# Kernel optimization log

Measured on AMD Instinct MI355X. Metric: run time of the kernel, lower is better.

## Reference

```python
import jax, jax.numpy as jnp
import numpy as np

IMG_H, IMG_W = 16, 16
N = IMG_H * IMG_W              # 256 tokens
HEADS = 8
HEAD_DIM = 32
INNER = HEADS * HEAD_DIM       # 256
IN_CH = 256
OUT_CH = 256
BATCH = 64
SCALE = HEAD_DIM ** -0.5


def _make_relative_index():
    # Mirrors the torch buffer construction exactly.
    coords = np.stack(np.meshgrid(np.arange(IMG_H), np.arange(IMG_W), indexing='ij'))
    coords = coords.reshape(2, -1)                      # (2, N)
    rel = coords[:, :, None] - coords[:, None, :]       # (2, N, N)
    rel[0] += IMG_H - 1
    rel[1] += IMG_W - 1
    rel[0] *= 2 * IMG_W - 1
    idx = rel.sum(0).reshape(-1)                        # (N*N,) values in [0, (2H-1)(2W-1))
    return idx.astype(np.int32)


def setup_inputs() -> dict:
    key = jax.random.key(0)
    k1, k2, k3, k4, k5 = jax.random.split(key, 5)
    x = jax.random.normal(k1, (BATCH, N, IN_CH), dtype=jnp.float32)
    w_qkv = jax.random.normal(k2, (IN_CH, 3 * INNER), dtype=jnp.float32) * 0.02
    bias_table = jax.random.normal(k3, ((2 * IMG_H - 1) * (2 * IMG_W - 1), HEADS), dtype=jnp.float32) * 0.02
    w_out = jax.random.normal(k4, (INNER, OUT_CH), dtype=jnp.float32) * 0.02
    b_out = jax.random.normal(k5, (OUT_CH,), dtype=jnp.float32) * 0.02
    rel_index = jnp.asarray(_make_relative_index())
    return {"x": x, "w_qkv": w_qkv, "bias_table": bias_table,
            "w_out": w_out, "b_out": b_out, "rel_index": rel_index}


def reference(x, w_qkv, bias_table, w_out, b_out, rel_index):
    b, n, _ = x.shape
    qkv = x @ w_qkv                                     # (b, n, 3*inner)
    q, k, v = jnp.split(qkv, 3, axis=-1)
    def heads(t):
        return t.reshape(b, n, HEADS, HEAD_DIM).transpose(0, 2, 1, 3)  # (b, h, n, d)
    q, k, v = heads(q), heads(k), heads(v)
    dots = jnp.einsum('bhid,bhjd->bhij', q, k) * SCALE  # (b, h, n, n)
    # gather relative position bias: (n*n, h) -> (1, h, n, n)
    rel_bias = bias_table[rel_index].reshape(n, n, HEADS).transpose(2, 0, 1)[None]
    attn = jax.nn.softmax(dots + rel_bias, axis=-1)
    out = jnp.einsum('bhij,bhjd->bhid', attn, v)        # (b, h, n, d)
    out = out.transpose(0, 2, 1, 3).reshape(b, n, INNER)
    return out @ w_out + b_out
```

## Files before the change

kernel.cpp:

```cpp
#include <hip/hip_runtime.h>
#include <hip/hip_bf16.h>

typedef __bf16 bfv8 __attribute__((ext_vector_type(8)));
typedef float f32x4 __attribute__((ext_vector_type(4)));
typedef unsigned short u16;
typedef unsigned int u32;
typedef u16 u16x8 __attribute__((ext_vector_type(8)));

__device__ __forceinline__ float bf2f(u16 u){ union{u32 i; float f;} x; x.i=(u32)u<<16; return x.f; }
__device__ __forceinline__ u16 f2bf(float f){ union{float f; u32 i;} x; x.f=f; u32 i=x.i; return (u16)((i + 0x7FFFu + ((i>>16)&1u))>>16); }

__device__ __forceinline__ void gl16(const void* g, void* l){
  __builtin_amdgcn_global_load_lds((const __attribute__((address_space(1))) unsigned int*)g,
                                   (__attribute__((address_space(3))) unsigned int*)l, 16, 0, 0);
}

__global__ __launch_bounds__(256) void prep_k(const float* __restrict__ x, u16* __restrict__ xb,
                                              const float* __restrict__ w_qkv, u16* __restrict__ wT,
                                              const float* __restrict__ w_out, u16* __restrict__ woT,
                                              const float* __restrict__ bt, const int* __restrict__ ridx,
                                              u16* __restrict__ biasp2){
  __shared__ u16 tile[32][34];
  const int bid = blockIdx.x, tid = threadIdx.x;
  if (bid < 2048){
    int i = (bid*256 + tid)*8;
    float4 a = *(const float4*)&x[i];
    float4 b = *(const float4*)&x[i+4];
    u16 r[8] = { f2bf(a.x),f2bf(a.y),f2bf(a.z),f2bf(a.w), f2bf(b.x),f2bf(b.y),f2bf(b.z),f2bf(b.w) };
    *(int4*)&xb[i] = *(int4*)r;
  } else if (bid < 2048+192){
    int b2 = bid - 2048;
    int c0 = (b2 % 24)*32, r0 = (b2/24)*32;
    int tx = tid & 31, ty = tid >> 5;
    #pragma unroll
    for(int dy=0; dy<32; dy+=8) tile[ty+dy][tx] = f2bf(w_qkv[(size_t)(r0+ty+dy)*768 + (c0+tx)]);
    __syncthreads();
    #pragma unroll
    for(int dy=0; dy<32; dy+=8) wT[(size_t)(c0+ty+dy)*256 + (r0+tx)] = tile[tx][ty+dy];
  } else if (bid < 2048+192+64){
    int b3 = bid - (2048+192);
    int c0 = (b3 & 7)*32, r0 = (b3 >> 3)*32;
    int tx = tid & 31, ty = tid >> 5;
    #pragma unroll
    for(int dy=0; dy<32; dy+=8) tile[ty+dy][tx] = f2bf(w_out[(size_t)(r0+ty+dy)*256 + (c0+tx)]);
    __syncthreads();
    #pragma unroll
    for(int dy=0; dy<32; dy+=8) woT[(size_t)(c0+ty+dy)*256 + (r0+tx)] = tile[tx][ty+dy];
  } else {
    const float L2E = 1.4426950408889634f;
    int idx = (bid - (2048+192+64))*256 + tid;
    int e = idx & 7, ch = (idx>>3)&7, lane = (idx>>6)&63, rb = (idx>>12)&15, h = (idx>>16)&7;
    int ll = lane & 15, lg = lane >> 4;
    int tj = ch*2 + (e>>2), r = e & 3;
    int q = rb*16 + ll, k = 16*tj + 4*lg + r;
    biasp2[idx] = f2bf(bt[ridx[q*256 + k]*8 + h] * L2E);
  }
}

template<bool BIAS, typename OUT, int TM>
__global__ __launch_bounds__(256) void gemm_k(const u16* __restrict__ A, const u16* __restrict__ Bt,
                         const float* __restrict__ bias, OUT* __restrict__ C, int M, int N, int K){
  constexpr int MI = TM/32;
  __shared__ u16 As[TM*64];
  __shared__ u16 Bs[128*64];
  const int tid = threadIdx.x, lane = tid & 63, wv = tid >> 6;
  const int lg = lane >> 4, ll = lane & 15;
  const int wr = (wv >> 1)*(TM/2), wc = (wv & 1)*64;
  const size_t m0 = (size_t)blockIdx.x*TM;
  const int n0 = blockIdx.y*128;
  const int lrow = lane >> 3, lcol = (lane & 7)*8;
  f32x4 acc[MI][4] = {};
  for(int k0=0; k0<K; k0+=64){
    #pragma unroll
    for(int c=0;c<MI;++c){
      int rowbase = (wv*MI + c)*8;
      gl16(&A[(m0 + rowbase + lrow)*(size_t)K + k0 + lcol], &As[rowbase*64]);
    }
    #pragma unroll
    for(int c=0;c<4;++c){
      int rowbase = (wv*4 + c)*8;
      gl16(&Bt[(size_t)(n0 + rowbase + lrow)*K + k0 + lcol], &Bs[rowbase*64]);
    }
    __syncthreads();
    bfv8 af[MI][2], bf[4][2];
    #pragma unroll
    for(int i=0;i<MI;++i)
      #pragma unroll
      for(int kh=0;kh<2;++kh) af[i][kh] = *(const bfv8*)&As[(wr+16*i+ll)*64 + kh*32 + lg*8];
    #pragma unroll
    for(int j=0;j<4;++j)
      #pragma unroll
      for(int kh=0;kh<2;++kh) bf[j][kh] = *(const bfv8*)&Bs[(wc+16*j+ll)*64 + kh*32 + lg*8];
    #pragma unroll
    for(int kh=0;kh<2;++kh)
      #pragma unroll
      for(int i=0;i<MI;++i)
        #pragma unroll
        for(int j=0;j<4;++j)
          acc[i][j] = __builtin_amdgcn_mfma_f32_16x16x32_bf16(af[i][kh], bf[j][kh], acc[i][j], 0,0,0);
    __syncthreads();
  }
  #pragma unroll
  for(int i=0;i<MI;++i)
    #pragma unroll
    for(int j=0;j<4;++j){
      int col = n0 + wc + 16*j + ll;
      float bv = 0.f;
      if (BIAS) bv = bias[col];
      #pragma unroll
      for(int r=0;r<4;++r){
        size_t row = m0 + wr + 16*i + lg*4 + r;
        float v = acc[i][j][r] + bv;
        if constexpr (sizeof(OUT) == 2) C[row*(size_t)N + col] = f2bf(v);
        else                            C[row*(size_t)N + col] = v;
      }
    }
}

__global__ __launch_bounds__(512) void attn_k(const u16* __restrict__ qkv, const u16* __restrict__ biasp2, u16* __restrict__ attnb){
  __shared__ u16 Ks[256*40];
  __shared__ u16 Vt[32*264];
  const int i = blockIdx.x;
  const int b = i & 63, h = i >> 6;
  const int tid = threadIdx.x, lane = tid & 63, wv = tid >> 6;
  const int lg = lane >> 4, ll = lane & 15;
  const u16* qb = qkv + (size_t)b*256*768;
  #pragma unroll
  for(int p=0;p<2;++p){
    int ch = tid + p*512;
    int j = ch >> 2, d8 = (ch & 3)*8;
    *(int4*)&Ks[j*40 + d8] = *(const int4*)&qb[(size_t)j*768 + 256 + h*32 + d8];
  }
  #pragma unroll
  for(int it=0; it<8; ++it){
    int e = tid + it*512;
    int j = e >> 4, dp = (e & 15)*2;
    int jp = ((j>>5)<<5) + 8*((j>>2)&3) + 4*((j>>4)&1) + (j&3);
    u32 v = *(const u32*)&qb[(size_t)j*768 + 512 + h*32 + dp];
    Vt[dp*264 + jp]     = (u16)(v & 0xffffu);
    Vt[(dp+1)*264 + jp] = (u16)(v >> 16);
  }
  __syncthreads();
  const float SCALE2 = 0.17677669529663687f * 1.4426950408889634f;
  const f32x4 zero = {0.f,0.f,0.f,0.f};
  #pragma unroll 1
  for(int iter=0; iter<2; ++iter){
    const int q0 = iter*128 + wv*16;
    const u16* bp = biasp2 + ((((size_t)h*16 + (q0>>4))*64 + lane) << 6);
    u16x8 bias[8];
    #pragma unroll
    for(int g=0; g<8; ++g) bias[g] = *(const u16x8*)&bp[g*8];
    bfv8 qf = *(const bfv8*)&qb[(size_t)(q0+ll)*768 + h*32 + lg*8];
    f32x4 s[16];
    #pragma unroll
    for(int tj=0;tj<16;++tj){
      bfv8 kf = *(const bfv8*)&Ks[(16*tj+ll)*40 + lg*8];
      s[tj] = __builtin_amdgcn_mfma_f32_16x16x32_bf16(kf, qf, zero, 0,0,0);
    }
    f32x4 sm = {0.f,0.f,0.f,0.f};
    #pragma unroll
    for(int tj=0;tj<16;++tj){
      #pragma unroll
      for(int r=0;r<4;++r){
        float p = exp2f(fmaf(s[tj][r], SCALE2, bf2f(bias[tj>>1][4*(tj&1)+r])));
        s[tj][r] = p;
        sm[r] += p;
      }
    }
    float sum = sm[0]+sm[1]+sm[2]+sm[3];
    sum += __shfl_xor(sum,16);
    sum += __shfl_xor(sum,32);
    float rinv = 1.0f/sum;
    u32 pk[16][2];
    #pragma unroll
    for(int tj=0;tj<16;++tj){
      asm("v_cvt_pk_bf16_f32 %0, %1, %2" : "=v"(pk[tj][0]) : "v"(s[tj][0]), "v"(s[tj][1]));
      asm("v_cvt_pk_bf16_f32 %0, %1, %2" : "=v"(pk[tj][1]) : "v"(s[tj][2]), "v"(s[tj][3]));
    }
    f32x4 o[2] = {zero, zero};
    #pragma unroll
    for(int c=0;c<8;++c){
      union { u32 u[4]; bfv8 v; } pu;
      pu.u[0] = pk[2*c][0]; pu.u[1] = pk[2*c][1]; pu.u[2] = pk[2*c+1][0]; pu.u[3] = pk[2*c+1][1];
      bfv8 pf = pu.v;
      #pragma unroll
      for(int td=0;td<2;++td){
        bfv8 vf = *(const bfv8*)&Vt[(16*td+ll)*264 + 32*c + lg*8];
        o[td] = __builtin_amdgcn_mfma_f32_16x16x32_bf16(pf, vf, o[td], 0,0,0);
      }
    }
    #pragma unroll
    for(int td=0;td<2;++td)
      #pragma unroll
      for(int r=0;r<4;++r){
        float rl = __shfl(rinv, 4*lg + r);
        int row = q0 + 4*lg + r;
        attnb[((size_t)b*256 + row)*256 + h*32 + 16*td + ll] = f2bf(o[td][r]*rl);
      }
  }
}

extern "C" void kernel_launch(void* const* d_in, const int* in_sizes, int n_in,
                              void* d_out, int out_size, void* d_ws, size_t ws_size,
                              hipStream_t stream) {
  const float* x     = (const float*)d_in[0];
  const float* w_qkv = (const float*)d_in[1];
  const float* btab  = (const float*)d_in[2];
  const float* w_out = (const float*)d_in[3];
  const float* b_out = (const float*)d_in[4];
  const int*   ridx  = (const int*)d_in[5];
  float* out = (float*)d_out;

  char* ws = (char*)d_ws;
  size_t off = 0;
  u16*   xb     = (u16*)(ws + off); off += (size_t)64*256*256*2;
  u16*   wT     = (u16*)(ws + off); off += (size_t)768*256*2;
  u16*   woT    = (u16*)(ws + off); off += (size_t)256*256*2;
  u16*   biasp2 = (u16*)(ws + off); off += (size_t)524288*2;
  u16*   qkvb   = (u16*)(ws + off); off += (size_t)64*256*768*2;
  u16*   attnb  = (u16*)(ws + off); off += (size_t)64*256*256*2;

  prep_k<<<2048+192+64+2048,256,0,stream>>>(x, xb, w_qkv, wT, w_out, woT, btab, ridx, biasp2);
  gemm_k<false,u16,64><<<dim3(256,6),256,0,stream>>>(xb, wT, nullptr, qkvb, 16384, 768, 256);
  attn_k<<<512,512,0,stream>>>(qkvb, biasp2, attnb);
  gemm_k<true,float,32><<<dim3(512,2),256,0,stream>>>(attnb, woT, b_out, out, 16384, 256, 256);
}
```

Baseline: 56.66 us.

## Compute softmax row sums via MFMA with ones and prefetch bias/Q before K/V staging

The attention kernel now issues the global loads for both query tiles' bias and Q fragments before staging K and V into shared memory, so their latency overlaps the LDS fill. The softmax denominator is taken from an extra MFMA against a vector of bf16 ones instead of a VALU sum plus cross-lane shuffles, which also makes it use the same bf16-rounded probabilities as the PV product. It adds s_setprio around the MFMA phases and sets a minimum-blocks launch bound. The cost is extra registers for the doubled prefetched state and a possible occupancy or spill risk from the launch bound.

Measured after the change: 61.95 us. 1.09x slower.

```diff
diff --git a/kernel.cpp b/kernel.cpp
--- a/kernel.cpp
+++ b/kernel.cpp
@@ -117,7 +117,7 @@
     }
 }
 
-__global__ __launch_bounds__(512) void attn_k(const u16* __restrict__ qkv, const u16* __restrict__ biasp2, u16* __restrict__ attnb){
+__global__ __launch_bounds__(512,4) void attn_k(const u16* __restrict__ qkv, const u16* __restrict__ biasp2, u16* __restrict__ attnb){
   __shared__ u16 Ks[256*40];
   __shared__ u16 Vt[32*264];
   const int i = blockIdx.x;
@@ -125,6 +125,14 @@
   const int tid = threadIdx.x, lane = tid & 63, wv = tid >> 6;
   const int lg = lane >> 4, ll = lane & 15;
   const u16* qb = qkv + (size_t)b*256*768;
+  const int q00 = wv*16, q01 = 128 + wv*16;
+  const u16* bp0 = biasp2 + ((((size_t)h*16 + (q00>>4))*64 + lane) << 6);
+  const u16* bp1 = biasp2 + ((((size_t)h*16 + (q01>>4))*64 + lane) << 6);
+  u16x8 bias0[8], bias1[8];
+  #pragma unroll
+  for(int g=0; g<8; ++g){ bias0[g] = *(const u16x8*)&bp0[g*8]; bias1[g] = *(const u16x8*)&bp1[g*8]; }
+  bfv8 qf0 = *(const bfv8*)&qb[(size_t)(q00+ll)*768 + h*32 + lg*8];
+  bfv8 qf1 = *(const bfv8*)&qb[(size_t)(q01+ll)*768 + h*32 + lg*8];
   #pragma unroll
   for(int p=0;p<2;++p){
     int ch = tid + p*512;
@@ -143,34 +151,23 @@
   __syncthreads();
   const float SCALE2 = 0.17677669529663687f * 1.4426950408889634f;
   const f32x4 zero = {0.f,0.f,0.f,0.f};
-  #pragma unroll 1
-  for(int iter=0; iter<2; ++iter){
-    const int q0 = iter*128 + wv*16;
-    const u16* bp = biasp2 + ((((size_t)h*16 + (q0>>4))*64 + lane) << 6);
-    u16x8 bias[8];
-    #pragma unroll
-    for(int g=0; g<8; ++g) bias[g] = *(const u16x8*)&bp[g*8];
-    bfv8 qf = *(const bfv8*)&qb[(size_t)(q0+ll)*768 + h*32 + lg*8];
+  union { u16 u[8]; bfv8 v; } one8;
+  #pragma unroll
+  for(int t=0;t<8;++t) one8.u[t] = 0x3F80;
+  auto process = [&](int q0, const u16x8* bias, bfv8 qf){
     f32x4 s[16];
+    __builtin_amdgcn_s_setprio(1);
     #pragma unroll
     for(int tj=0;tj<16;++tj){
       bfv8 kf = *(const bfv8*)&Ks[(16*tj+ll)*40 + lg*8];
       s[tj] = __builtin_amdgcn_mfma_f32_16x16x32_bf16(kf, qf, zero, 0,0,0);
     }
-    f32x4 sm = {0.f,0.f,0.f,0.f};
-    #pragma unroll
-    for(int tj=0;tj<16;++tj){
-      #pragma unroll
-      for(int r=0;r<4;++r){
-        float p = exp2f(fmaf(s[tj][r], SCALE2, bf2f(bias[tj>>1][4*(tj&1)+r])));
-        s[tj][r] = p;
-        sm[r] += p;
-      }
-    }
-    float sum = sm[0]+sm[1]+sm[2]+sm[3];
-    sum += __shfl_xor(sum,16);
-    sum += __shfl_xor(sum,32);
-    float rinv = 1.0f/sum;
+    __builtin_amdgcn_s_setprio(0);
+    #pragma unroll
+    for(int tj=0;tj<16;++tj)
+      #pragma unroll
+      for(int r=0;r<4;++r)
+        s[tj][r] = exp2f(fmaf(s[tj][r], SCALE2, bf2f(bias[tj>>1][4*(tj&1)+r])));
     u32 pk[16][2];
     #pragma unroll
     for(int tj=0;tj<16;++tj){
@@ -178,6 +175,8 @@
       asm("v_cvt_pk_bf16_f32 %0, %1, %2" : "=v"(pk[tj][1]) : "v"(s[tj][2]), "v"(s[tj][3]));
     }
     f32x4 o[2] = {zero, zero};
+    f32x4 o2 = zero;
+    __builtin_amdgcn_s_setprio(1);
     #pragma unroll
     for(int c=0;c<8;++c){
       union { u32 u[4]; bfv8 v; } pu;
@@ -188,16 +187,19 @@
         bfv8 vf = *(const bfv8*)&Vt[(16*td+ll)*264 + 32*c + lg*8];
         o[td] = __builtin_amdgcn_mfma_f32_16x16x32_bf16(pf, vf, o[td], 0,0,0);
       }
-    }
-    #pragma unroll
-    for(int td=0;td<2;++td)
-      #pragma unroll
-      for(int r=0;r<4;++r){
-        float rl = __shfl(rinv, 4*lg + r);
-        int row = q0 + 4*lg + r;
-        attnb[((size_t)b*256 + row)*256 + h*32 + 16*td + ll] = f2bf(o[td][r]*rl);
-      }
-  }
+      o2 = __builtin_amdgcn_mfma_f32_16x16x32_bf16(pf, one8.v, o2, 0,0,0);
+    }
+    __builtin_amdgcn_s_setprio(0);
+    #pragma unroll
+    for(int r=0;r<4;++r){
+      float rl = 1.0f/o2[r];
+      int row = q0 + 4*lg + r;
+      attnb[((size_t)b*256 + row)*256 + h*32 + ll]      = f2bf(o[0][r]*rl);
+      attnb[((size_t)b*256 + row)*256 + h*32 + 16 + ll] = f2bf(o[1][r]*rl);
+    }
+  };
+  process(q00, bias0, qf0);
+  process(q01, bias1, qf1);
 }
 
 extern "C" void kernel_launch(void* const* d_in, const int* in_sizes, int n_in,
```
